# Performance work log

Measured on AMD Instinct MI355X. Metric: run time of the kernel, lower is better.

## Reference

```python
import jax, jax.numpy as jnp
import numpy as np
from jax import lax

B, H, W = 2, 256, 256
K = 7
K2 = K * K
IN_CH = 32 * 2 + 81  # 145


def _conv(x, w, b):
    y = lax.conv_general_dilated(x, w, (1, 1), 'SAME', dimension_numbers=('NCHW', 'OIHW', 'NCHW'))
    return y + b[None, :, None, None]


def _lrelu(x):
    return jnp.where(x >= 0, x, 0.1 * x)


def _predictor(x, w1, b1, w2, b2, w3, b3, wo, bo, ww, bw):
    f = _lrelu(_conv(x, w1, b1))
    f = _lrelu(_conv(f, w2, b2))
    f = _lrelu(_conv(f, w3, b3))
    offsets = _conv(f, wo, bo)                     # (B, 2*K2, H, W)
    weights = jax.nn.softmax(_conv(f, ww, bw), 1)  # (B, K2, H, W)
    return offsets, weights


def _sample(image, offsets, weights):
    b, c, h, w = image.shape
    k2 = weights.shape[1]
    off = offsets.reshape(b, k2, 2, h, w)
    dx, dy = off[:, :, 0], off[:, :, 1]
    gy, gx = jnp.meshgrid(jnp.arange(h, dtype=image.dtype), jnp.arange(w, dtype=image.dtype), indexing='ij')
    sx = gx[None, None] + dx  # (b,k2,h,w)
    sy = gy[None, None] + dy
    # Original normalizes with 2*s/(n-1)-1 (align_corners=True formula) but calls
    # grid_sample(align_corners=False): pixel coord = ((g+1)*n - 1)/2 = s*n/(n-1) - 0.5.
    # padding_mode='border' == clamp coord to [0, n-1] before bilinear.
    px = jnp.clip(sx * (w / (w - 1.0)) - 0.5, 0.0, w - 1.0)
    py = jnp.clip(sy * (h / (h - 1.0)) - 0.5, 0.0, h - 1.0)
    x0 = jnp.floor(px)
    y0 = jnp.floor(py)
    fx = (px - x0)[:, None]  # (b,1,k2,h,w)
    fy = (py - y0)[:, None]
    x0i = x0.astype(jnp.int32)
    y0i = y0.astype(jnp.int32)
    x1i = jnp.minimum(x0i + 1, w - 1)
    y1i = jnp.minimum(y0i + 1, h - 1)
    img = image.reshape(b, c, h * w)

    def gather(yi, xi):
        idx = (yi * w + xi).reshape(b, 1, k2 * h * w)
        return jnp.take_along_axis(img, idx, axis=2).reshape(b, c, k2, h, w)

    v00 = gather(y0i, x0i)
    v01 = gather(y0i, x1i)
    v10 = gather(y1i, x0i)
    v11 = gather(y1i, x1i)
    sampled = (v00 * (1 - fx) * (1 - fy) + v01 * fx * (1 - fy)
               + v10 * (1 - fx) * fy + v11 * fx * fy)
    return jnp.einsum('bkhw,bckhw->bchw', weights, sampled)


def setup_inputs() -> dict:
    key = jax.random.key(0)
    ks = iter(jax.random.split(key, 64))

    def nrm(shape, s=1.0):
        return jax.random.normal(next(ks), shape, jnp.float32) * s

    off0 = np.array([[j - K // 2, i - K // 2] for i in range(K) for j in range(K)],
                    np.float32).reshape(-1)  # interleaved (dx, dy) default grid

    def pred_params(p):
        return {
            p + '_w1': nrm((256, IN_CH, 3, 3), 0.02), p + '_b1': jnp.zeros((256,), jnp.float32),
            p + '_w2': nrm((256, 256, 3, 3), 0.02), p + '_b2': jnp.zeros((256,), jnp.float32),
            p + '_w3': nrm((128, 256, 3, 3), 0.02), p + '_b3': jnp.zeros((128,), jnp.float32),
            p + '_wo': nrm((2 * K2, 128, 3, 3), 0.01), p + '_bo': jnp.asarray(off0),
            p + '_ww': nrm((K2, 128, 3, 3), 0.02), p + '_bw': jnp.full((K2,), 1.0 / K2, jnp.float32),
        }

    inp = {
        'frame1': nrm((B, 3, H, W)),
        'frame2': nrm((B, 3, H, W)),
        'feat1': nrm((B, 32, H, W)),
        'feat2': nrm((B, 32, H, W)),
        'corr': nrm((B, 81, H, W)),
    }
    inp.update(pred_params('k1'))
    inp.update(pred_params('k2'))
    inp['bl_w1'] = nrm((64, IN_CH, 3, 3), 0.02)
    inp['bl_b1'] = jnp.zeros((64,), jnp.float32)
    inp['bl_w2'] = nrm((1, 64, 3, 3), 0.02)
    inp['bl_b2'] = jnp.zeros((1,), jnp.float32)
    return inp


def reference(frame1, frame2, feat1, feat2, corr,
              k1_w1, k1_b1, k1_w2, k1_b2, k1_w3, k1_b3, k1_wo, k1_bo, k1_ww, k1_bw,
              k2_w1, k2_b1, k2_w2, k2_b2, k2_w3, k2_b3, k2_wo, k2_bo, k2_ww, k2_bw,
              bl_w1, bl_b1, bl_w2, bl_b2):
    combined = jnp.concatenate([feat1, feat2, corr], axis=1)  # (B,145,H,W)
    off1, wt1 = _predictor(combined, k1_w1, k1_b1, k1_w2, k1_b2, k1_w3, k1_b3, k1_wo, k1_bo, k1_ww, k1_bw)
    off2, wt2 = _predictor(combined, k2_w1, k2_b1, k2_w2, k2_b2, k2_w3, k2_b3, k2_wo, k2_bo, k2_ww, k2_bw)
    s1 = _sample(frame1, off1, wt1)
    s2 = _sample(frame2, off2, wt2)
    blend = jax.nn.sigmoid(_conv(_lrelu(_conv(combined, bl_w1, bl_b1)), bl_w2, bl_b2))
    output = blend * s1 + (1.0 - blend) * s2
    return (output, blend, off1, off2, wt1, wt2)
```

## Files before the change

kernel.cpp:

```cpp
#include <hip/hip_runtime.h>


static constexpr int HW  = 65536;
static constexpr int WID = 256;
static constexpr int PAD = 66564;

using f32x16 = __attribute__((ext_vector_type(16))) float;
using s16x8  = __attribute__((ext_vector_type(8))) short;

__device__ __forceinline__ unsigned short f2b(float f) {
    unsigned u = __builtin_bit_cast(unsigned, f);
    u += 0x7fffu + ((u >> 16) & 1u);
    return (unsigned short)(u >> 16);
}
__device__ __forceinline__ float b2f(unsigned short h) {
    unsigned u = ((unsigned)h) << 16;
    return __builtin_bit_cast(float, u);
}

template <int N> __device__ __forceinline__ void vm_wait() {
    asm volatile("s_waitcnt vmcnt(%0)" :: "n"(N) : "memory");
}

__global__ void pack_x(const float* __restrict__ feat1, const float* __restrict__ feat2,
                       const float* __restrict__ corr, unsigned short* __restrict__ Xc) {
    int idx = blockIdx.x * 256 + threadIdx.x;
    int g  = idx >> 17;
    int bp = idx & (2 * HW - 1);
    int b  = bp >> 16, p = bp & 65535;
    unsigned short v[8];
#pragma unroll
    for (int j = 0; j < 8; ++j) {
        int c = g * 8 + j;
        float val = 0.f;
        if (c < 32)       val = feat1[(size_t)(b * 32 + c) * HW + p];
        else if (c < 64)  val = feat2[(size_t)(b * 32 + (c - 32)) * HW + p];
        else if (c < 145) val = corr [(size_t)(b * 81 + (c - 64)) * HW + p];
        v[j] = f2b(val);
    }
    uint4 u;
    u.x = v[0] | ((unsigned)v[1] << 16);
    u.y = v[2] | ((unsigned)v[3] << 16);
    u.z = v[4] | ((unsigned)v[5] << 16);
    u.w = v[6] | ((unsigned)v[7] << 16);
    int y = p >> 8, x = p & 255;
    size_t cell = (size_t)b * PAD + (size_t)(y + 1) * 258 + (x + 1);
    *reinterpret_cast<uint4*>(Xc + cell * 160 + g * 8) = u;
}

__global__ void pack_w(const float* __restrict__ W, unsigned short* __restrict__ Wp,
                       int OC, int IC, int OCP, int KC) {
    int idx = blockIdx.x * 256 + threadIdx.x;
    int total = 9 * KC * 4 * OCP * 8;
    if (idx >= total) return;
    int i8 = idx & 7;  int r = idx >> 3;
    int oc = r % OCP;  r /= OCP;
    int g  = r & 3;    r >>= 2;
    int kb = r % KC;   int s = r / KC;
    int ic = kb * 32 + g * 8 + i8;
    float v = (oc < OC && ic < IC) ? W[((size_t)(oc * IC + ic)) * 9 + s] : 0.f;
    Wp[idx] = f2b(v);
}

__global__ void zero_border(unsigned short* __restrict__ buf, int C) {
    int idx = blockIdx.x * 256 + threadIdx.x;
    int G = C >> 3;
    int total = 2 * 1028 * G;
    if (idx >= total) return;
    int gi = idx % G; int r = idx / G;
    int ci = r % 1028; int b = r / 1028;
    int row, col;
    if (ci < 258)      { row = 0;            col = ci; }
    else if (ci < 516) { row = 257;          col = ci - 258; }
    else if (ci < 772) { row = ci - 516 + 1; col = 0; }
    else               { row = ci - 772 + 1; col = 257; }
    *reinterpret_cast<uint4*>(buf + ((size_t)b * PAD + row * 258 + col) * C + gi * 8) =
        make_uint4(0u, 0u, 0u, 0u);
}

template <int ICP, int OCP, int OCT, int MODE>
__global__ __launch_bounds__(OCP / 128 * 256, 2) void conv3x3(
    const unsigned short* __restrict__ X,
    const uint4* __restrict__ Wp,
    const float* __restrict__ bias,
    unsigned short* __restrict__ outB,
    float* __restrict__ outF)
{
    constexpr int NT  = OCP / 128 * 256;
    constexpr int KC  = ICP / 32;
    constexpr int XGR = 1536;
    constexpr int WGR = OCP * 4;
    constexpr int XIT = XGR / NT;
    __shared__ uint4 lds[2 * XGR + 2 * WGR];

    const int t = threadIdx.x;
    const int lane = t & 63, wv = t >> 6;
    const int wm = wv >> 2, wn = wv & 3;
    const int l31 = lane & 31, hi = lane >> 5;

    const int bid  = blockIdx.x;
    const int work = ((bid & 7) << 6) | (bid >> 3);
    const int bb = work >> 8;
    const int tt = work & 255;
    const int tr = tt >> 3, tc = tt & 7;

    auto stage_x = [&](int kb, int slot) {
#pragma unroll
        for (int it = 0; it < XIT; ++it) {
            int G = it * NT + t;
            int g = G / 384;
            int cell = G - g * 384;
            cell = min(cell, 339);
            int rr = cell / 34, cc = cell - rr * 34;
            const unsigned short* src = X +
                ((size_t)bb * PAD + (size_t)(tr * 8 + rr) * 258 + tc * 32 + cc) * ICP +
                kb * 32 + g * 8;
            __builtin_amdgcn_global_load_lds(
                (const __attribute__((address_space(1))) unsigned int*)src,
                (__attribute__((address_space(3))) unsigned int*)&lds[slot * XGR + it * NT + (t & ~63)],
                16, 0, 0);
        }
    };
    auto stage_w = [&](int s, int kb, int slot) {
        const uint4* src = Wp + (size_t)(s * KC + kb) * WGR;
#pragma unroll
        for (int it = 0; it < 2; ++it) {
            __builtin_amdgcn_global_load_lds(
                (const __attribute__((address_space(1))) unsigned int*)(src + it * NT + t),
                (__attribute__((address_space(3))) unsigned int*)&lds[2 * XGR + slot * WGR + it * NT + (t & ~63)],
                16, 0, 0);
        }
    };

    f32x16 acc[4][2] = {};

    stage_x(0, 0);
    stage_w(0, 0, 0);
    vm_wait<0>();
    __builtin_amdgcn_s_barrier();

    int ph = 0;
    for (int kb = 0; kb < KC; ++kb) {
        const int xb = (kb & 1) * XGR;
#pragma unroll
        for (int s = 0; s < 9; ++s) {
            const int wcur = 2 * XGR + (ph & 1) * WGR;
            const bool lastPhase = (kb == KC - 1) && (s == 8);
            if (s < 8) {
                stage_w(s + 1, kb, (ph & 1) ^ 1);
            } else if (kb + 1 < KC) {
                stage_w(0, kb + 1, (ph & 1) ^ 1);
                stage_x(kb + 1, (kb & 1) ^ 1);
            }
            if (lastPhase)      vm_wait<0>();
            else if (s == 8)    vm_wait<2 + XIT>();
            else                vm_wait<2>();
            __builtin_amdgcn_s_barrier();

            const int dy = s / 3, dx = s - 3 * (s / 3);
            __builtin_amdgcn_s_setprio(1);
#pragma unroll
            for (int ks = 0; ks < 2; ++ks) {
                uint4 a[4], bq[2];
#pragma unroll
                for (int fm = 0; fm < 4; ++fm)
                    a[fm] = lds[wcur + (ks * 2 + hi) * OCP + wm * 128 + fm * 32 + l31];
#pragma unroll
                for (int fn = 0; fn < 2; ++fn)
                    bq[fn] = lds[xb + (ks * 2 + hi) * 384 + (wn * 2 + fn + dy) * 34 + dx + l31];
#pragma unroll
                for (int fm = 0; fm < 4; ++fm)
#pragma unroll
                    for (int fn = 0; fn < 2; ++fn)
                        acc[fm][fn] = __builtin_amdgcn_mfma_f32_32x32x16_bf16(
                            __builtin_bit_cast(s16x8, a[fm]),
                            __builtin_bit_cast(s16x8, bq[fn]),
                            acc[fm][fn], 0, 0, 0);
            }
            __builtin_amdgcn_s_setprio(0);
            __builtin_amdgcn_s_barrier();
            ph ^= 1;
        }
    }

#pragma unroll
    for (int fm = 0; fm < 4; ++fm) {
#pragma unroll
        for (int fn = 0; fn < 2; ++fn) {
            const int prow = wn * 2 + fn;
            if (MODE == 0) {
                const size_t cellp = (size_t)bb * PAD + (size_t)(tr * 8 + prow + 1) * 258 + tc * 32 + l31 + 1;
#pragma unroll
                for (int q = 0; q < 4; ++q) {
                    const int oc0 = wm * 128 + fm * 32 + q * 8 + hi * 4;
                    if (oc0 < OCT) {
                        float4 bv = *reinterpret_cast<const float4*>(bias + oc0);
                        const float* bvp = reinterpret_cast<const float*>(&bv);
                        unsigned short o[4];
#pragma unroll
                        for (int j = 0; j < 4; ++j) {
                            float r = acc[fm][fn][q * 4 + j] + bvp[j];
                            r = (r >= 0.f) ? r : 0.1f * r;
                            o[j] = f2b(r);
                        }
                        uint2 pk;
                        pk.x = o[0] | ((unsigned)o[1] << 16);
                        pk.y = o[2] | ((unsigned)o[3] << 16);
                        *reinterpret_cast<uint2*>(outB + cellp * OCT + oc0) = pk;
                    }
                }
            } else {
                const int py = tr * 8 + prow, px = tc * 32 + l31;
#pragma unroll
                for (int q = 0; q < 4; ++q) {
                    const int oc0 = wm * 128 + fm * 32 + q * 8 + hi * 4;
#pragma unroll
                    for (int j = 0; j < 4; ++j) {
                        const int oc = oc0 + j;
                        if (oc < OCT)
                            outF[((size_t)bb * OCT + oc) * HW + py * WID + px] =
                                acc[fm][fn][q * 4 + j] + bias[oc];
                    }
                }
            }
        }
    }
}

__global__ void softmax49(float* __restrict__ L) {
    int idx = blockIdx.x * 256 + threadIdx.x;
    int b = idx >> 16, p = idx & 65535;
    float* lp = L + (size_t)b * 49 * HW + p;
    float v[49];
    float mx = -1e30f;
#pragma unroll
    for (int k = 0; k < 49; ++k) { v[k] = lp[(size_t)k * HW]; mx = fmaxf(mx, v[k]); }
    float sum = 0.f;
#pragma unroll
    for (int k = 0; k < 49; ++k) { v[k] = expf(v[k] - mx); sum += v[k]; }
    float inv = 1.f / sum;
#pragma unroll
    for (int k = 0; k < 49; ++k) lp[(size_t)k * HW] = v[k] * inv;
}

__global__ void blend2k(const unsigned short* __restrict__ Fb, const float* __restrict__ W2,
                        const float* __restrict__ B2, float* __restrict__ blendOut) {
    int idx = blockIdx.x * 256 + threadIdx.x;
    int b = idx >> 16, p = idx & 65535, y = p >> 8, x = p & 255;
    float acc = B2[0];
#pragma unroll
    for (int ry = 0; ry < 3; ++ry) {
#pragma unroll
        for (int rx = 0; rx < 3; ++rx) {
            const unsigned short* fp = Fb + ((size_t)b * PAD + (size_t)(y + ry) * 258 + (x + rx)) * 64;
#pragma unroll
            for (int g = 0; g < 8; ++g) {
                uint4 u = *reinterpret_cast<const uint4*>(fp + g * 8);
                unsigned w[4] = {u.x, u.y, u.z, u.w};
#pragma unroll
                for (int h = 0; h < 4; ++h) {
                    int c = g * 8 + h * 2;
                    acc += b2f((unsigned short)(w[h] & 0xffffu)) * W2[(c)     * 9 + ry * 3 + rx];
                    acc += b2f((unsigned short)(w[h] >> 16))     * W2[(c + 1) * 9 + ry * 3 + rx];
                }
            }
        }
    }
    blendOut[idx] = 1.f / (1.f + expf(-acc));
}

__device__ __forceinline__ void sample_accum(const float* __restrict__ img,
                                             const float* __restrict__ off,
                                             const float* __restrict__ wt,
                                             int x, int y, float s[3]) {
    for (int k = 0; k < 49; ++k) {
        float dx = off[(size_t)(2 * k) * HW];
        float dy = off[(size_t)(2 * k + 1) * HW];
        float w  = wt [(size_t)k * HW];
        float px = ((float)x + dx) * (256.f / 255.f) - 0.5f;
        float py = ((float)y + dy) * (256.f / 255.f) - 0.5f;
        px = fminf(fmaxf(px, 0.f), 255.f);
        py = fminf(fmaxf(py, 0.f), 255.f);
        float x0f = floorf(px), y0f = floorf(py);
        float fx = px - x0f, fy = py - y0f;
        int x0 = (int)x0f, y0 = (int)y0f;
        int x1 = min(x0 + 1, 255), y1 = min(y0 + 1, 255);
        float w00 = (1.f - fx) * (1.f - fy), w01 = fx * (1.f - fy);
        float w10 = (1.f - fx) * fy,         w11 = fx * fy;
#pragma unroll
        for (int c = 0; c < 3; ++c) {
            const float* ip = img + (size_t)c * HW;
            float v = ip[y0 * WID + x0] * w00 + ip[y0 * WID + x1] * w01 +
                      ip[y1 * WID + x0] * w10 + ip[y1 * WID + x1] * w11;
            s[c] += w * v;
        }
    }
}

__global__ void sample_final(const float* __restrict__ fr1, const float* __restrict__ fr2,
                             const float* __restrict__ off1, const float* __restrict__ off2,
                             const float* __restrict__ wt1, const float* __restrict__ wt2,
                             const float* __restrict__ blend, float* __restrict__ out) {
    int idx = blockIdx.x * 256 + threadIdx.x;
    int b = idx >> 16, p = idx & 65535, y = p >> 8, x = p & 255;
    float s1[3] = {0.f, 0.f, 0.f}, s2[3] = {0.f, 0.f, 0.f};
    sample_accum(fr1 + (size_t)b * 3 * HW, off1 + (size_t)b * 98 * HW + p,
                 wt1 + (size_t)b * 49 * HW + p, x, y, s1);
    sample_accum(fr2 + (size_t)b * 3 * HW, off2 + (size_t)b * 98 * HW + p,
                 wt2 + (size_t)b * 49 * HW + p, x, y, s2);
    float bl = blend[idx];
#pragma unroll
    for (int c = 0; c < 3; ++c)
        out[(size_t)(b * 3 + c) * HW + p] = bl * s1[c] + (1.f - bl) * s2[c];
}

extern "C" void kernel_launch(void* const* d_in, const int* in_sizes, int n_in,
                              void* d_out, int out_size, void* d_ws, size_t ws_size,
                              hipStream_t stream) {
    (void)in_sizes; (void)n_in; (void)out_size; (void)ws_size;
    const float* frame1 = (const float*)d_in[0];
    const float* frame2 = (const float*)d_in[1];
    const float* feat1  = (const float*)d_in[2];
    const float* feat2  = (const float*)d_in[3];
    const float* corr   = (const float*)d_in[4];
    const float* Wsrc[2][5];
    const float* Bsrc[2][5];
    for (int pdx = 0; pdx < 2; ++pdx) {
        int base = 5 + pdx * 10;
        for (int l = 0; l < 5; ++l) {
            Wsrc[pdx][l] = (const float*)d_in[base + 2 * l];
            Bsrc[pdx][l] = (const float*)d_in[base + 2 * l + 1];
        }
    }
    const float* bl_w1 = (const float*)d_in[25];
    const float* bl_b1 = (const float*)d_in[26];
    const float* bl_w2 = (const float*)d_in[27];
    const float* bl_b2 = (const float*)d_in[28];

    float* out      = (float*)d_out;
    float* out_bl   = out + 393216;
    float* out_off[2] = {out + 524288,   out + 13369344};
    float* out_wt [2] = {out + 26214400, out + 32636928};

    char* ws = (char*)d_ws;
    size_t o = 0;
    auto alloc = [&](size_t bytes) { char* p = ws + o; o += (bytes + 255) & ~(size_t)255; return p; };
    unsigned short* Xc   = (unsigned short*)alloc((size_t)2 * PAD * 160 * 2);
    unsigned short* bufA = (unsigned short*)alloc((size_t)2 * PAD * 256 * 2);
    unsigned short* bufB = (unsigned short*)alloc((size_t)2 * PAD * 256 * 2);
    unsigned short *WpC1[2], *WpC2[2], *WpC3[2], *WpCo[2], *WpCw[2];
    for (int pdx = 0; pdx < 2; ++pdx) {
        WpC1[pdx] = (unsigned short*)alloc((size_t)9 * 256 * 160 * 2);
        WpC2[pdx] = (unsigned short*)alloc((size_t)9 * 256 * 256 * 2);
        WpC3[pdx] = (unsigned short*)alloc((size_t)9 * 128 * 256 * 2);
        WpCo[pdx] = (unsigned short*)alloc((size_t)9 * 128 * 128 * 2);
        WpCw[pdx] = (unsigned short*)alloc((size_t)9 * 128 * 128 * 2);
    }
    unsigned short* WpBl = (unsigned short*)alloc((size_t)9 * 128 * 160 * 2);

    auto packw = [&](const float* W, unsigned short* Wp, int OC, int IC, int OCP, int ICP) {
        int total = 9 * OCP * ICP;
        pack_w<<<(total + 255) / 256, 256, 0, stream>>>(W, Wp, OC, IC, OCP, ICP / 32);
    };
    auto zb = [&](unsigned short* buf, int C) {
        int total = 2 * 1028 * (C / 8);
        zero_border<<<(total + 255) / 256, 256, 0, stream>>>(buf, C);
    };

    zb(Xc, 160);
    pack_x<<<(2 * HW * 20) / 256, 256, 0, stream>>>(feat1, feat2, corr, Xc);
    for (int pdx = 0; pdx < 2; ++pdx) {
        packw(Wsrc[pdx][0], WpC1[pdx], 256, 145, 256, 160);
        packw(Wsrc[pdx][1], WpC2[pdx], 256, 256, 256, 256);
        packw(Wsrc[pdx][2], WpC3[pdx], 128, 256, 128, 256);
        packw(Wsrc[pdx][3], WpCo[pdx],  98, 128, 128, 128);
        packw(Wsrc[pdx][4], WpCw[pdx],  49, 128, 128, 128);
    }
    packw(bl_w1, WpBl, 64, 145, 128, 160);
    zb(bufB, 256);

    for (int pdx = 0; pdx < 2; ++pdx) {
        zb(bufA, 256);
        conv3x3<160, 256, 256, 0><<<512, 512, 0, stream>>>(
            Xc, (const uint4*)WpC1[pdx], Bsrc[pdx][0], bufA, nullptr);
        conv3x3<256, 256, 256, 0><<<512, 512, 0, stream>>>(
            bufA, (const uint4*)WpC2[pdx], Bsrc[pdx][1], bufB, nullptr);
        zb(bufA, 128);
        conv3x3<256, 128, 128, 0><<<512, 256, 0, stream>>>(
            bufB, (const uint4*)WpC3[pdx], Bsrc[pdx][2], bufA, nullptr);
        conv3x3<128, 128, 98, 1><<<512, 256, 0, stream>>>(
            bufA, (const uint4*)WpCo[pdx], Bsrc[pdx][3], nullptr, out_off[pdx]);
        conv3x3<128, 128, 49, 1><<<512, 256, 0, stream>>>(
            bufA, (const uint4*)WpCw[pdx], Bsrc[pdx][4], nullptr, out_wt[pdx]);
        softmax49<<<512, 256, 0, stream>>>(out_wt[pdx]);
    }

    zb(bufB, 64);
    conv3x3<160, 128, 64, 0><<<512, 256, 0, stream>>>(
        Xc, (const uint4*)WpBl, bl_b1, bufB, nullptr);
    blend2k<<<512, 256, 0, stream>>>(bufB, bl_w2, bl_b2, out_bl);

    sample_final<<<512, 256, 0, stream>>>(frame1, frame2, out_off[0], out_off[1],
                                          out_wt[0], out_wt[1], out_bl, out);
}
```

Baseline: 1.275 ms.

## Split wide convs across output-channel grid blocks and pack frames as float4 for sampling

The 256-output-channel convolutions now launch 256-thread blocks over a 2D grid, with each block handling 128 output channels. Weight staging indexes into the packed weights by output-channel offset, which doubles block count and lowers per-block resources for better occupancy, at the cost of reloading the input tile twice. Separately, a new kernel packs both RGB frames into an interleaved float4 layout in scratch. The bilinear sampler can then fetch all channels of a tap with one 16-byte load instead of three scattered loads.

After: 1.289 ms. No clear change (+1.1%).

```diff
diff --git a/kernel.cpp b/kernel.cpp
--- a/kernel.cpp
+++ b/kernel.cpp
@@ -6,6 +6,7 @@
 static constexpr int PAD = 66564;
 
 using f32x16 = __attribute__((ext_vector_type(16))) float;
+using f32x4  = __attribute__((ext_vector_type(4))) float;
 using s16x8  = __attribute__((ext_vector_type(8))) short;
 
 __device__ __forceinline__ unsigned short f2b(float f) {
@@ -78,25 +79,25 @@
         make_uint4(0u, 0u, 0u, 0u);
 }
 
-template <int ICP, int OCP, int OCT, int MODE>
-__global__ __launch_bounds__(OCP / 128 * 256, 2) void conv3x3(
+template <int ICP, int OCF, int OCT, int MODE>
+__global__ __launch_bounds__(256, 2) void conv3x3(
     const unsigned short* __restrict__ X,
     const uint4* __restrict__ Wp,
     const float* __restrict__ bias,
     unsigned short* __restrict__ outB,
     float* __restrict__ outF)
 {
-    constexpr int NT  = OCP / 128 * 256;
+    constexpr int NT  = 256;
     constexpr int KC  = ICP / 32;
     constexpr int XGR = 1536;
-    constexpr int WGR = OCP * 4;
+    constexpr int WGR = 512;
     constexpr int XIT = XGR / NT;
     __shared__ uint4 lds[2 * XGR + 2 * WGR];
 
     const int t = threadIdx.x;
-    const int lane = t & 63, wv = t >> 6;
-    const int wm = wv >> 2, wn = wv & 3;
+    const int lane = t & 63, wn = t >> 6;
     const int l31 = lane & 31, hi = lane >> 5;
+    const int ocOff = blockIdx.y * 128;
 
     const int bid  = blockIdx.x;
     const int work = ((bid & 7) << 6) | (bid >> 3);
@@ -122,11 +123,13 @@
         }
     };
     auto stage_w = [&](int s, int kb, int slot) {
-        const uint4* src = Wp + (size_t)(s * KC + kb) * WGR;
 #pragma unroll
         for (int it = 0; it < 2; ++it) {
+            int G = it * NT + t;
+            int g = G >> 7, oc = G & 127;
+            const uint4* src = Wp + ((size_t)(s * KC + kb) * 4 + g) * OCF + ocOff + oc;
             __builtin_amdgcn_global_load_lds(
-                (const __attribute__((address_space(1))) unsigned int*)(src + it * NT + t),
+                (const __attribute__((address_space(1))) unsigned int*)src,
                 (__attribute__((address_space(3))) unsigned int*)&lds[2 * XGR + slot * WGR + it * NT + (t & ~63)],
                 16, 0, 0);
         }
@@ -164,7 +167,7 @@
                 uint4 a[4], bq[2];
 #pragma unroll
                 for (int fm = 0; fm < 4; ++fm)
-                    a[fm] = lds[wcur + (ks * 2 + hi) * OCP + wm * 128 + fm * 32 + l31];
+                    a[fm] = lds[wcur + (ks * 2 + hi) * 128 + fm * 32 + l31];
 #pragma unroll
                 for (int fn = 0; fn < 2; ++fn)
                     bq[fn] = lds[xb + (ks * 2 + hi) * 384 + (wn * 2 + fn + dy) * 34 + dx + l31];
@@ -192,9 +195,9 @@
                 const size_t cellp = (size_t)bb * PAD + (size_t)(tr * 8 + prow + 1) * 258 + tc * 32 + l31 + 1;
 #pragma unroll
                 for (int q = 0; q < 4; ++q) {
-                    const int oc0 = wm * 128 + fm * 32 + q * 8 + hi * 4;
-                    if (oc0 < OCT) {
-                        float4 bv = *reinterpret_cast<const float4*>(bias + oc0);
+                    const int goc = ocOff + fm * 32 + q * 8 + hi * 4;
+                    if (goc < OCT) {
+                        float4 bv = *reinterpret_cast<const float4*>(bias + goc);
                         const float* bvp = reinterpret_cast<const float*>(&bv);
                         unsigned short o[4];
 #pragma unroll
@@ -206,17 +209,16 @@
                         uint2 pk;
                         pk.x = o[0] | ((unsigned)o[1] << 16);
                         pk.y = o[2] | ((unsigned)o[3] << 16);
-                        *reinterpret_cast<uint2*>(outB + cellp * OCT + oc0) = pk;
+                        *reinterpret_cast<uint2*>(outB + cellp * OCT + goc) = pk;
                     }
                 }
             } else {
                 const int py = tr * 8 + prow, px = tc * 32 + l31;
 #pragma unroll
                 for (int q = 0; q < 4; ++q) {
-                    const int oc0 = wm * 128 + fm * 32 + q * 8 + hi * 4;
 #pragma unroll
                     for (int j = 0; j < 4; ++j) {
-                        const int oc = oc0 + j;
+                        const int oc = ocOff + fm * 32 + q * 8 + hi * 4 + j;
                         if (oc < OCT)
                             outF[((size_t)bb * OCT + oc) * HW + py * WID + px] =
                                 acc[fm][fn][q * 4 + j] + bias[oc];
@@ -269,10 +271,24 @@
     blendOut[idx] = 1.f / (1.f + expf(-acc));
 }
 
-__device__ __forceinline__ void sample_accum(const float* __restrict__ img,
-                                             const float* __restrict__ off,
-                                             const float* __restrict__ wt,
-                                             int x, int y, float s[3]) {
+__global__ void pack_frames(const float* __restrict__ f1, const float* __restrict__ f2,
+                            f32x4* __restrict__ Ff) {
+    int idx = blockIdx.x * 256 + threadIdx.x;
+    int fr = idx >> 17; int bp = idx & (2 * HW - 1);
+    const float* src = fr ? f2 : f1;
+    int b = bp >> 16, p = bp & 65535;
+    f32x4 v;
+    v[0] = src[(size_t)(b * 3 + 0) * HW + p];
+    v[1] = src[(size_t)(b * 3 + 1) * HW + p];
+    v[2] = src[(size_t)(b * 3 + 2) * HW + p];
+    v[3] = 0.f;
+    Ff[(size_t)fr * 2 * HW + bp] = v;
+}
+
+__device__ __forceinline__ void sample_accum4(const f32x4* __restrict__ img,
+                                              const float* __restrict__ off,
+                                              const float* __restrict__ wt,
+                                              int x, int y, f32x4& s) {
     for (int k = 0; k < 49; ++k) {
         float dx = off[(size_t)(2 * k) * HW];
         float dy = off[(size_t)(2 * k + 1) * HW];
@@ -285,29 +301,25 @@
         float fx = px - x0f, fy = py - y0f;
         int x0 = (int)x0f, y0 = (int)y0f;
         int x1 = min(x0 + 1, 255), y1 = min(y0 + 1, 255);
-        float w00 = (1.f - fx) * (1.f - fy), w01 = fx * (1.f - fy);
-        float w10 = (1.f - fx) * fy,         w11 = fx * fy;
-#pragma unroll
-        for (int c = 0; c < 3; ++c) {
-            const float* ip = img + (size_t)c * HW;
-            float v = ip[y0 * WID + x0] * w00 + ip[y0 * WID + x1] * w01 +
-                      ip[y1 * WID + x0] * w10 + ip[y1 * WID + x1] * w11;
-            s[c] += w * v;
-        }
-    }
-}
-
-__global__ void sample_final(const float* __restrict__ fr1, const float* __restrict__ fr2,
+        const f32x4* r0 = img + y0 * WID;
+        const f32x4* r1 = img + y1 * WID;
+        f32x4 v = (1.f - fy) * ((1.f - fx) * r0[x0] + fx * r0[x1]) +
+                  fy         * ((1.f - fx) * r1[x0] + fx * r1[x1]);
+        s += w * v;
+    }
+}
+
+__global__ void sample_final(const f32x4* __restrict__ Ff,
                              const float* __restrict__ off1, const float* __restrict__ off2,
                              const float* __restrict__ wt1, const float* __restrict__ wt2,
                              const float* __restrict__ blend, float* __restrict__ out) {
     int idx = blockIdx.x * 256 + threadIdx.x;
     int b = idx >> 16, p = idx & 65535, y = p >> 8, x = p & 255;
-    float s1[3] = {0.f, 0.f, 0.f}, s2[3] = {0.f, 0.f, 0.f};
-    sample_accum(fr1 + (size_t)b * 3 * HW, off1 + (size_t)b * 98 * HW + p,
-                 wt1 + (size_t)b * 49 * HW + p, x, y, s1);
-    sample_accum(fr2 + (size_t)b * 3 * HW, off2 + (size_t)b * 98 * HW + p,
-                 wt2 + (size_t)b * 49 * HW + p, x, y, s2);
+    f32x4 s1 = {0.f, 0.f, 0.f, 0.f}, s2 = {0.f, 0.f, 0.f, 0.f};
+    sample_accum4(Ff + (size_t)b * HW, off1 + (size_t)b * 98 * HW + p,
+                  wt1 + (size_t)b * 49 * HW + p, x, y, s1);
+    sample_accum4(Ff + (size_t)(2 + b) * HW, off2 + (size_t)b * 98 * HW + p,
+                  wt2 + (size_t)b * 49 * HW + p, x, y, s2);
     float bl = blend[idx];
 #pragma unroll
     for (int c = 0; c < 3; ++c)
@@ -357,6 +369,7 @@
         WpCw[pdx] = (unsigned short*)alloc((size_t)9 * 128 * 128 * 2);
     }
     unsigned short* WpBl = (unsigned short*)alloc((size_t)9 * 128 * 160 * 2);
+    f32x4* Ff = (f32x4*)bufA;
 
     auto packw = [&](const float* W, unsigned short* Wp, int OC, int IC, int OCP, int ICP) {
         int total = 9 * OCP * ICP;
@@ -381,25 +394,26 @@
 
     for (int pdx = 0; pdx < 2; ++pdx) {
         zb(bufA, 256);
-        conv3x3<160, 256, 256, 0><<<512, 512, 0, stream>>>(
+        conv3x3<160, 256, 256, 0><<<dim3(512, 2), 256, 0, stream>>>(
             Xc, (const uint4*)WpC1[pdx], Bsrc[pdx][0], bufA, nullptr);
-        conv3x3<256, 256, 256, 0><<<512, 512, 0, stream>>>(
+        conv3x3<256, 256, 256, 0><<<dim3(512, 2), 256, 0, stream>>>(
             bufA, (const uint4*)WpC2[pdx], Bsrc[pdx][1], bufB, nullptr);
         zb(bufA, 128);
-        conv3x3<256, 128, 128, 0><<<512, 256, 0, stream>>>(
+        conv3x3<256, 128, 128, 0><<<dim3(512, 1), 256, 0, stream>>>(
             bufB, (const uint4*)WpC3[pdx], Bsrc[pdx][2], bufA, nullptr);
-        conv3x3<128, 128, 98, 1><<<512, 256, 0, stream>>>(
+        conv3x3<128, 128, 98, 1><<<dim3(512, 1), 256, 0, stream>>>(
             bufA, (const uint4*)WpCo[pdx], Bsrc[pdx][3], nullptr, out_off[pdx]);
-        conv3x3<128, 128, 49, 1><<<512, 256, 0, stream>>>(
+        conv3x3<128, 128, 49, 1><<<dim3(512, 1), 256, 0, stream>>>(
             bufA, (const uint4*)WpCw[pdx], Bsrc[pdx][4], nullptr, out_wt[pdx]);
         softmax49<<<512, 256, 0, stream>>>(out_wt[pdx]);
     }
 
     zb(bufB, 64);
-    conv3x3<160, 128, 64, 0><<<512, 256, 0, stream>>>(
+    conv3x3<160, 128, 64, 0><<<dim3(512, 1), 256, 0, stream>>>(
         Xc, (const uint4*)WpBl, bl_b1, bufB, nullptr);
     blend2k<<<512, 256, 0, stream>>>(bufB, bl_w2, bl_b2, out_bl);
 
-    sample_final<<<512, 256, 0, stream>>>(frame1, frame2, out_off[0], out_off[1],
+    pack_frames<<<(4 * HW) / 256, 256, 0, stream>>>(frame1, frame2, Ff);
+    sample_final<<<512, 256, 0, stream>>>(Ff, out_off[0], out_off[1],
                                           out_wt[0], out_wt[1], out_bl, out);
 }
```
